# Kernel optimization log

Measured on AMD Instinct MI355X. Metric: run time of the kernel, lower is better.

## Reference

```python
import jax, jax.numpy as jnp
import numpy as np

BN_EPS = 1e-5

def _batchnorm(z, gamma, beta):
    # training-mode BN over node axis, biased variance (matches torch normalization)
    mean = jnp.mean(z, axis=0)
    var = jnp.mean((z - mean) ** 2, axis=0)
    return (z - mean) * jax.lax.rsqrt(var + BN_EPS) * gamma + beta

def setup_inputs() -> dict:
    key = jax.random.key(0)
    N, E, D, L = 100000, 1000000, 128, 2
    ks = jax.random.split(key, 8)
    x = jax.random.normal(ks[0], (N, D), dtype=jnp.float32)
    edge_index = jax.random.randint(ks[1], (2, E), 0, N, dtype=jnp.int64)
    s = 1.0 / np.sqrt(D)
    W1 = jax.random.uniform(ks[2], (L, D, D), jnp.float32, -s, s)
    b1 = jax.random.uniform(ks[3], (L, D), jnp.float32, -s, s)
    W2 = jax.random.uniform(ks[4], (L, D, D), jnp.float32, -s, s)
    b2 = jax.random.uniform(ks[5], (L, D), jnp.float32, -s, s)
    g1 = jnp.ones((L, D), jnp.float32); bt1 = jnp.zeros((L, D), jnp.float32)
    g_out = jnp.ones((L, D), jnp.float32); bt_out = jnp.zeros((L, D), jnp.float32)
    eps = jnp.zeros((L,), jnp.float32)  # GIN eps, init 0
    return {"x": x, "edge_index": edge_index, "W1": W1, "b1": b1, "g1": g1,
            "bt1": bt1, "W2": W2, "b2": b2, "eps": eps, "g_out": g_out, "bt_out": bt_out}

def reference(x, edge_index, W1, b1, g1, bt1, W2, b2, eps, g_out, bt_out):
    N = x.shape[0]
    L = W1.shape[0]
    src, dst = edge_index[0], edge_index[1]
    h = x
    for l in range(L):
        # message: relu(x_j) gathered along edges; aggregate: scatter-add to dst
        msg = jax.nn.relu(h[src])                                  # [E, D]
        aggr = jax.ops.segment_sum(msg, dst, num_segments=N)       # [N, D]
        z = (1.0 + eps[l]) * h + aggr
        # GINConv MLP: Linear -> BN -> ReLU -> Linear
        z = z @ W1[l].T + b1[l]
        z = jax.nn.relu(_batchnorm(z, g1[l], bt1[l]))
        z = z @ W2[l].T + b2[l]
        # outer per-layer BatchNorm
        z = _batchnorm(z, g_out[l], bt_out[l])
        if l < L - 1:
            z = jax.nn.relu(z)
        # dropout is identity in eval mode
        h = z
    return h
```

## Files before the change

kernel.cpp:

```cpp
#include <hip/hip_runtime.h>

typedef unsigned int u32;
typedef unsigned short u16;
typedef __attribute__((ext_vector_type(8))) short bf16x8;
typedef __attribute__((ext_vector_type(4))) float f32x4;

#define DF 128
#define NBUCK 256
#define BUCK_SHIFT 9
#define BUCK_SIZE 512
#define P2_CHUNK 4096
#define NCOPY 16
#define STATW (NCOPY * DF)

__device__ __forceinline__ float bf2f(u32 h) { return __uint_as_float(h << 16); }
__device__ __forceinline__ u16 f2bf(float f) {
  u32 u = __float_as_uint(f);
  u32 r = (u + 0x7fffu + ((u >> 16) & 1u)) >> 16;
  return (u16)r;
}
__device__ __forceinline__ u32 pack2(float a, float b) {
  return (u32)f2bf(a) | ((u32)f2bf(b) << 16);
}

__global__ void k_cvt_f32_bf16(const float* __restrict__ in, u16* __restrict__ out, int n4) {
  int i = blockIdx.x * blockDim.x + threadIdx.x;
  if (i >= n4) return;
  float4 v = ((const float4*)in)[i];
  ((uint2*)out)[i] = make_uint2(pack2(v.x, v.y), pack2(v.z, v.w));
}

__global__ __launch_bounds__(256) void k_p1(const int* __restrict__ dst,
                                            int* __restrict__ bucketCount, int E) {
  __shared__ int h[NBUCK];
  int t = threadIdx.x;
  h[t] = 0;
  __syncthreads();
  for (int e = blockIdx.x * 256 + t; e < E; e += gridDim.x * 256)
    atomicAdd(&h[((u32)dst[e]) >> BUCK_SHIFT], 1);
  __syncthreads();
  if (h[t]) atomicAdd(&bucketCount[t], h[t]);
}

__global__ __launch_bounds__(256) void k_pscan(const int* __restrict__ bucketCount,
                                               int* __restrict__ bucketStart,
                                               int* __restrict__ bucketCursor,
                                               int* __restrict__ rowptr, int N, int E) {
  __shared__ int sh[NBUCK];
  int t = threadIdx.x;
  int c = bucketCount[t];
  sh[t] = c;
  __syncthreads();
  for (int o = 1; o < 256; o <<= 1) {
    int v = (t >= o) ? sh[t - o] : 0;
    __syncthreads();
    sh[t] += v;
    __syncthreads();
  }
  int excl = sh[t] - c;
  bucketStart[t] = excl;
  bucketCursor[t] = excl;
  if (t == 255) { bucketStart[256] = sh[255]; rowptr[N] = E; }
}

__global__ __launch_bounds__(256) void k_p2(const int* __restrict__ src,
                                            const int* __restrict__ dst,
                                            int* __restrict__ bucketCursor,
                                            uint2* __restrict__ part, int E) {
  __shared__ int h[NBUCK], hs[NBUCK], base[NBUCK];
  __shared__ int total;
  __shared__ uint2 buf[P2_CHUNK];
  int t = threadIdx.x;
  int e0 = blockIdx.x * P2_CHUNK;
  h[t] = 0;
  __syncthreads();
  int myb[16], myr[16];
  uint2 mye[16];
  #pragma unroll
  for (int k = 0; k < 16; k++) {
    int e = e0 + k * 256 + t;
    myb[k] = -1;
    if (e < E) {
      int s = src[e], d = dst[e];
      mye[k] = make_uint2((u32)s, (u32)d);
      myb[k] = ((u32)d) >> BUCK_SHIFT;
      myr[k] = atomicAdd(&h[myb[k]], 1);
    }
  }
  __syncthreads();
  int hc = h[t];
  hs[t] = hc;
  __syncthreads();
  for (int o = 1; o < 256; o <<= 1) {
    int v = (t >= o) ? hs[t - o] : 0;
    __syncthreads();
    hs[t] += v;
    __syncthreads();
  }
  if (t == 255) total = hs[255];
  int excl = hs[t] - hc;
  base[t] = hc ? atomicAdd(&bucketCursor[t], hc) : 0;
  __syncthreads();
  hs[t] = excl;
  __syncthreads();
  #pragma unroll
  for (int k = 0; k < 16; k++)
    if (myb[k] >= 0) buf[hs[myb[k]] + myr[k]] = mye[k];
  __syncthreads();
  int tot = total;
  for (int i = t; i < tot; i += 256) {
    uint2 ed = buf[i];
    int b = ed.y >> BUCK_SHIFT;
    part[base[b] + (i - hs[b])] = ed;
  }
}

__global__ __launch_bounds__(256) void k_p3(const uint2* __restrict__ part,
                                            const int* __restrict__ bucketStart,
                                            int* __restrict__ rowptr,
                                            int* __restrict__ adj, int N) {
  __shared__ int deg[BUCK_SIZE], cur[BUCK_SIZE], psum[256];
  int b = blockIdx.x, t = threadIdx.x;
  int nodeBase = b << BUCK_SHIFT;
  int eb = bucketStart[b], ee = bucketStart[b + 1];
  deg[t] = 0; deg[t + 256] = 0;
  __syncthreads();
  for (int e = eb + t; e < ee; e += 256)
    atomicAdd(&deg[(int)part[e].y - nodeBase], 1);
  __syncthreads();
  int a0 = deg[2 * t], a1 = deg[2 * t + 1];
  psum[t] = a0 + a1;
  __syncthreads();
  for (int o = 1; o < 256; o <<= 1) {
    int v = (t >= o) ? psum[t - o] : 0;
    __syncthreads();
    psum[t] += v;
    __syncthreads();
  }
  int basep = psum[t] - (a0 + a1);
  int p0 = eb + basep, p1 = eb + basep + a0;
  cur[2 * t] = p0; cur[2 * t + 1] = p1;
  int n0 = nodeBase + 2 * t, n1 = nodeBase + 2 * t + 1;
  if (n0 < N) rowptr[n0] = p0;
  if (n1 < N) rowptr[n1] = p1;
  __syncthreads();
  for (int e = eb + t; e < ee; e += 256) {
    uint2 ed = part[e];
    int pos = atomicAdd(&cur[(int)ed.y - nodeBase], 1);
    adj[pos] = (int)ed.x;
  }
}

__global__ void k_aggr(const u16* __restrict__ hself, const u16* __restrict__ hmsg,
                       const int* __restrict__ rowptr, const int* __restrict__ adj,
                       const float* __restrict__ epsArr, int layer, int doRelu,
                       u16* __restrict__ z, int N) {
  int wid = (blockIdx.x * blockDim.x + threadIdx.x) >> 6;
  if (wid >= N) return;
  int lane = threadIdx.x & 63;
  int g = lane >> 4, f = lane & 15;
  const uint4* hs4 = (const uint4*)hself;
  const uint4* hm4 = (const uint4*)hmsg;
  float e1 = 1.0f + epsArr[layer];

  float acc[8];
  #pragma unroll
  for (int k = 0; k < 8; k++) acc[k] = 0.0f;

  if (g == 0) {
    uint4 v = hs4[(size_t)wid * 16 + f];
    u32 w[4] = {v.x, v.y, v.z, v.w};
    #pragma unroll
    for (int k = 0; k < 4; k++) {
      acc[2 * k]     = e1 * __uint_as_float(w[k] << 16);
      acc[2 * k + 1] = e1 * __uint_as_float(w[k] & 0xffff0000u);
    }
  }

  int b = rowptr[wid], e = rowptr[wid + 1];
  for (int p = b; p < e; p += 8) {
    int i0 = p + g, i1 = p + 4 + g;
    uint4 v0 = make_uint4(0, 0, 0, 0), v1 = make_uint4(0, 0, 0, 0);
    if (i0 < e) v0 = hm4[(size_t)(u32)adj[i0] * 16 + f];
    if (i1 < e) v1 = hm4[(size_t)(u32)adj[i1] * 16 + f];
    u32 w0[4] = {v0.x, v0.y, v0.z, v0.w};
    u32 w1[4] = {v1.x, v1.y, v1.z, v1.w};
    if (doRelu) {
      #pragma unroll
      for (int k = 0; k < 4; k++) {
        u32 a = w0[k];
        if (a & 0x8000u)     a &= 0xffff0000u;
        if (a & 0x80000000u) a &= 0x0000ffffu;
        w0[k] = a;
        u32 bq = w1[k];
        if (bq & 0x8000u)     bq &= 0xffff0000u;
        if (bq & 0x80000000u) bq &= 0x0000ffffu;
        w1[k] = bq;
      }
    }
    #pragma unroll
    for (int k = 0; k < 4; k++) {
      acc[2 * k]     += __uint_as_float(w0[k] << 16);
      acc[2 * k + 1] += __uint_as_float(w0[k] & 0xffff0000u);
      acc[2 * k]     += __uint_as_float(w1[k] << 16);
      acc[2 * k + 1] += __uint_as_float(w1[k] & 0xffff0000u);
    }
  }

  #pragma unroll
  for (int k = 0; k < 8; k++) {
    acc[k] += __shfl_xor(acc[k], 16);
    acc[k] += __shfl_xor(acc[k], 32);
  }
  if (g == 0) {
    uint4 o = make_uint4(pack2(acc[0], acc[1]), pack2(acc[2], acc[3]),
                         pack2(acc[4], acc[5]), pack2(acc[6], acc[7]));
    ((uint4*)z)[(size_t)wid * 16 + f] = o;
  }
}

__global__ __launch_bounds__(256, 2) void k_gemm(
    const u16* __restrict__ A, const u16* __restrict__ W, const float* __restrict__ bias,
    const float* __restrict__ ain, const float* __restrict__ cin, int trans,
    float* __restrict__ statS, float* __restrict__ statQ,
    u16* __restrict__ out, int Nrows) {
  __shared__ u16 lA[4 * 8 * 64 * 8];
  __shared__ u16 lB[4 * 8 * 64 * 8];
  int tid = threadIdx.x;
  int rowBase = blockIdx.x * 128;

  #pragma unroll
  for (int cc = 0; cc < 8; cc++) {
    int c = tid + cc * 256;
    int lane = c & 63, rt = (c >> 6) & 7, kt = c >> 9;
    int m = lane & 15, quad = lane >> 4;
    int grow = rowBase + rt * 16 + m;
    int gk = kt * 32 + quad * 8;
    uint4 val = make_uint4(0, 0, 0, 0);
    if (grow < Nrows) val = *(const uint4*)(A + (size_t)grow * DF + gk);
    if (trans) {
      float4 av0 = *(const float4*)(ain + gk);
      float4 av1 = *(const float4*)(ain + gk + 4);
      float4 cv0 = *(const float4*)(cin + gk);
      float4 cv1 = *(const float4*)(cin + gk + 4);
      float f0 = fmaxf(fmaf(av0.x, bf2f(val.x & 0xffffu), cv0.x), 0.0f);
      float f1 = fmaxf(fmaf(av0.y, bf2f(val.x >> 16),     cv0.y), 0.0f);
      float f2 = fmaxf(fmaf(av0.z, bf2f(val.y & 0xffffu), cv0.z), 0.0f);
      float f3 = fmaxf(fmaf(av0.w, bf2f(val.y >> 16),     cv0.w), 0.0f);
      float f4 = fmaxf(fmaf(av1.x, bf2f(val.z & 0xffffu), cv1.x), 0.0f);
      float f5 = fmaxf(fmaf(av1.y, bf2f(val.z >> 16),     cv1.y), 0.0f);
      float f6 = fmaxf(fmaf(av1.z, bf2f(val.w & 0xffffu), cv1.z), 0.0f);
      float f7 = fmaxf(fmaf(av1.w, bf2f(val.w >> 16),     cv1.w), 0.0f);
      val = make_uint4(pack2(f0, f1), pack2(f2, f3), pack2(f4, f5), pack2(f6, f7));
    }
    ((uint4*)lA)[c] = val;
  }
  #pragma unroll
  for (int cc = 0; cc < 8; cc++) {
    int c = tid + cc * 256;
    int lane = c & 63, ct = (c >> 6) & 7, kt = c >> 9;
    int n = lane & 15, quad = lane >> 4;
    ((uint4*)lB)[c] = *(const uint4*)(W + (ct * 16 + n) * DF + kt * 32 + quad * 8);
  }
  __syncthreads();

  int lane = tid & 63, w = tid >> 6;
  int rq = w >> 1, cq = w & 1;
  f32x4 acc[4][4];
  #pragma unroll
  for (int i = 0; i < 4; i++)
    #pragma unroll
    for (int j = 0; j < 4; j++) acc[i][j] = (f32x4){0.f, 0.f, 0.f, 0.f};

  const bf16x8* pA = (const bf16x8*)lA;
  const bf16x8* pB = (const bf16x8*)lB;
  #pragma unroll
  for (int kt = 0; kt < 4; kt++) {
    bf16x8 af[4], bfr[4];
    #pragma unroll
    for (int i = 0; i < 4; i++) af[i] = pA[(kt * 8 + rq * 4 + i) * 64 + lane];
    #pragma unroll
    for (int j = 0; j < 4; j++) bfr[j] = pB[(kt * 8 + cq * 4 + j) * 64 + lane];
    #pragma unroll
    for (int i = 0; i < 4; i++)
      #pragma unroll
      for (int j = 0; j < 4; j++)
        acc[i][j] = __builtin_amdgcn_mfma_f32_16x16x32_bf16(af[i], bfr[j], acc[i][j], 0, 0, 0);
  }

  int mcol = lane & 15, quad = lane >> 4;
  float colS[4] = {0, 0, 0, 0}, colQ[4] = {0, 0, 0, 0};
  #pragma unroll
  for (int j = 0; j < 4; j++) {
    int col = (cq * 4 + j) * 16 + mcol;
    float bv = bias[col];
    #pragma unroll
    for (int i = 0; i < 4; i++) {
      int row0 = rowBase + (rq * 4 + i) * 16 + quad * 4;
      #pragma unroll
      for (int r = 0; r < 4; r++) {
        int row = row0 + r;
        if (row < Nrows) {
          float v = acc[i][j][r] + bv;
          out[(size_t)row * DF + col] = f2bf(v);
          colS[j] += v;
          colQ[j] += v * v;
        }
      }
    }
  }
  int copyOff = (blockIdx.x & (NCOPY - 1)) * DF;
  #pragma unroll
  for (int j = 0; j < 4; j++) {
    float s = colS[j], q = colQ[j];
    s += __shfl_xor(s, 16); q += __shfl_xor(q, 16);
    s += __shfl_xor(s, 32); q += __shfl_xor(q, 32);
    if (quad == 0) {
      int col = (cq * 4 + j) * 16 + mcol;
      atomicAdd(&statS[copyOff + col], s);
      atomicAdd(&statQ[copyOff + col], q);
    }
  }
}

__global__ void k_finalize(const float* __restrict__ s, const float* __restrict__ q,
                           const float* __restrict__ gamma, const float* __restrict__ beta,
                           float* __restrict__ a, float* __restrict__ c, int Nrows) {
  int t = threadIdx.x;
  if (t < DF) {
    float S = 0.f, Q = 0.f;
    #pragma unroll
    for (int i = 0; i < NCOPY; i++) { S += s[i * DF + t]; Q += q[i * DF + t]; }
    float inv_n = 1.0f / (float)Nrows;
    float mean = S * inv_n;
    float var = fmaxf(Q * inv_n - mean * mean, 0.0f);
    float iv = rsqrtf(var + 1e-5f);
    float av = gamma[t] * iv;
    a[t] = av;
    c[t] = beta[t] - mean * av;
  }
}

__global__ void k_bnapply_bf16(const u16* __restrict__ u, const float* __restrict__ a,
                               const float* __restrict__ c, u16* __restrict__ h, int n8, int relu) {
  int i = blockIdx.x * blockDim.x + threadIdx.x;
  if (i >= n8) return;
  int col = (i * 8) & 127;
  float4 a0 = *(const float4*)(a + col), a1v = *(const float4*)(a + col + 4);
  float4 c0 = *(const float4*)(c + col), c1v = *(const float4*)(c + col + 4);
  uint4 v = ((const uint4*)u)[i];
  float f0 = fmaf(a0.x, bf2f(v.x & 0xffffu), c0.x);
  float f1 = fmaf(a0.y, bf2f(v.x >> 16),     c0.y);
  float f2 = fmaf(a0.z, bf2f(v.y & 0xffffu), c0.z);
  float f3 = fmaf(a0.w, bf2f(v.y >> 16),     c0.w);
  float f4 = fmaf(a1v.x, bf2f(v.z & 0xffffu), c1v.x);
  float f5 = fmaf(a1v.y, bf2f(v.z >> 16),     c1v.y);
  float f6 = fmaf(a1v.z, bf2f(v.w & 0xffffu), c1v.z);
  float f7 = fmaf(a1v.w, bf2f(v.w >> 16),     c1v.w);
  if (relu) {
    f0 = fmaxf(f0, 0.f); f1 = fmaxf(f1, 0.f); f2 = fmaxf(f2, 0.f); f3 = fmaxf(f3, 0.f);
    f4 = fmaxf(f4, 0.f); f5 = fmaxf(f5, 0.f); f6 = fmaxf(f6, 0.f); f7 = fmaxf(f7, 0.f);
  }
  ((uint4*)h)[i] = make_uint4(pack2(f0, f1), pack2(f2, f3), pack2(f4, f5), pack2(f6, f7));
}

__global__ void k_bnapply_f32(const u16* __restrict__ u, const float* __restrict__ a,
                              const float* __restrict__ c, float* __restrict__ out, int n8) {
  int i = blockIdx.x * blockDim.x + threadIdx.x;
  if (i >= n8) return;
  int col = (i * 8) & 127;
  float4 a0 = *(const float4*)(a + col), a1v = *(const float4*)(a + col + 4);
  float4 c0 = *(const float4*)(c + col), c1v = *(const float4*)(c + col + 4);
  uint4 v = ((const uint4*)u)[i];
  float4 o0, o1;
  o0.x = fmaf(a0.x, bf2f(v.x & 0xffffu), c0.x);
  o0.y = fmaf(a0.y, bf2f(v.x >> 16),     c0.y);
  o0.z = fmaf(a0.z, bf2f(v.y & 0xffffu), c0.z);
  o0.w = fmaf(a0.w, bf2f(v.y >> 16),     c0.w);
  o1.x = fmaf(a1v.x, bf2f(v.z & 0xffffu), c1v.x);
  o1.y = fmaf(a1v.y, bf2f(v.z >> 16),     c1v.y);
  o1.z = fmaf(a1v.z, bf2f(v.w & 0xffffu), c1v.z);
  o1.w = fmaf(a1v.w, bf2f(v.w >> 16),     c1v.w);
  ((float4*)out)[i * 2] = o0;
  ((float4*)out)[i * 2 + 1] = o1;
}

extern "C" void kernel_launch(void* const* d_in, const int* in_sizes, int n_in,
                              void* d_out, int out_size, void* d_ws, size_t ws_size,
                              hipStream_t stream) {
  const float* x    = (const float*)d_in[0];
  const int*   ei   = (const int*)d_in[1];
  const float* W1   = (const float*)d_in[2];
  const float* b1   = (const float*)d_in[3];
  const float* g1   = (const float*)d_in[4];
  const float* bt1  = (const float*)d_in[5];
  const float* W2   = (const float*)d_in[6];
  const float* b2   = (const float*)d_in[7];
  const float* eps  = (const float*)d_in[8];
  const float* gout = (const float*)d_in[9];
  const float* btout= (const float*)d_in[10];

  int N = in_sizes[0] / DF;
  int E = in_sizes[1] / 2;
  int L = in_sizes[8];

  char* ws = (char*)d_ws;
  size_t off = 0;
  auto alloc = [&](size_t bytes) -> void* {
    void* p = ws + off;
    off += (bytes + 255) & ~(size_t)255;
    return p;
  };
  u16* Xb     = (u16*)alloc((size_t)N * DF * 2);
  u16* bufA   = (u16*)alloc((size_t)N * DF * 2);
  u16* bufB   = (u16*)alloc((size_t)N * DF * 2);
  int* rowptr = (int*)alloc((size_t)(N + 1) * 4);
  int* adj    = (int*)alloc((size_t)E * 4);
  uint2* part = (uint2*)alloc((size_t)E * 8);
  int* bCount = (int*)alloc(NBUCK * 4);
  int* bStart = (int*)alloc((NBUCK + 1) * 4);
  int* bCur   = (int*)alloc(NBUCK * 4);
  u16* W1b    = (u16*)alloc((size_t)L * DF * DF * 2);
  u16* W2b    = (u16*)alloc((size_t)L * DF * DF * 2);
  float* stats= (float*)alloc((size_t)L * 4 * STATW * 4);
  float* coefs= (float*)alloc((size_t)L * 4 * DF * 4);

  hipMemsetAsync(bCount, 0, NBUCK * 4, stream);
  hipMemsetAsync(stats, 0, (size_t)L * 4 * STATW * 4, stream);

  int n4x = N * DF / 4;
  k_cvt_f32_bf16<<<(n4x + 255) / 256, 256, 0, stream>>>(x, Xb, n4x);
  int n4w = L * DF * DF / 4;
  k_cvt_f32_bf16<<<(n4w + 255) / 256, 256, 0, stream>>>(W1, W1b, n4w);
  k_cvt_f32_bf16<<<(n4w + 255) / 256, 256, 0, stream>>>(W2, W2b, n4w);

  const int* srcI = ei;
  const int* dstI = ei + E;
  int nbuckets = (N + BUCK_SIZE - 1) >> BUCK_SHIFT;
  k_p1<<<512, 256, 0, stream>>>(dstI, bCount, E);
  k_pscan<<<1, 256, 0, stream>>>(bCount, bStart, bCur, rowptr, N, E);
  k_p2<<<(E + P2_CHUNK - 1) / P2_CHUNK, 256, 0, stream>>>(srcI, dstI, bCur, part, E);
  k_p3<<<nbuckets, 256, 0, stream>>>(part, bStart, rowptr, adj, N);

  int gblocks = (N + 127) / 128;
  int n8 = N * DF / 8;
  for (int l = 0; l < L; l++) {
    float* S1 = stats + (size_t)(l * 4 + 0) * STATW;
    float* Q1 = stats + (size_t)(l * 4 + 1) * STATW;
    float* S2 = stats + (size_t)(l * 4 + 2) * STATW;
    float* Q2 = stats + (size_t)(l * 4 + 3) * STATW;
    float* a1 = coefs + (size_t)(l * 4 + 0) * DF;
    float* c1 = coefs + (size_t)(l * 4 + 1) * DF;
    float* a2 = coefs + (size_t)(l * 4 + 2) * DF;
    float* c2 = coefs + (size_t)(l * 4 + 3) * DF;
    const u16* H = (l == 0) ? Xb : bufB;
    k_aggr<<<(N + 3) / 4, 256, 0, stream>>>(H, H, rowptr, adj, eps, l,
                                            (l == 0) ? 1 : 0, bufA, N);
    k_gemm<<<gblocks, 256, 0, stream>>>(bufA, W1b + l * DF * DF, b1 + l * DF,
                                        nullptr, nullptr, 0, S1, Q1, bufB, N);
    k_finalize<<<1, 128, 0, stream>>>(S1, Q1, g1 + l * DF, bt1 + l * DF, a1, c1, N);
    k_gemm<<<gblocks, 256, 0, stream>>>(bufB, W2b + l * DF * DF, b2 + l * DF,
                                        a1, c1, 1, S2, Q2, bufA, N);
    k_finalize<<<1, 128, 0, stream>>>(S2, Q2, gout + l * DF, btout + l * DF, a2, c2, N);
    if (l < L - 1) {
      k_bnapply_bf16<<<(n8 + 255) / 256, 256, 0, stream>>>(bufA, a2, c2, bufB, n8, 1);
    } else {
      k_bnapply_f32<<<(n8 + 255) / 256, 256, 0, stream>>>(bufA, a2, c2, (float*)d_out, n8);
    }
  }
}
```

Measured before the change: 436.9 us.

## Fuse BN finalize into consumers, drop GEMM LDS staging, merge conversions

The three f32-to-bf16 conversion launches are merged into one kernel. Each block of the downstream GEMM or BN-apply kernel now recomputes the BN coefficients from the partial sums, so the single-block finalize launches go away. The GEMM loads MFMA fragments straight from global memory instead of staging A and W through LDS, and occupancy is raised to 3 blocks. The aggregation accumulators become vector types. This trades launch count and LDS traffic for redundant per-block stat reduction and uncoalesced 16-byte fragment loads from global memory.

New measurement: 449.6 us. 1.03x slower.

```diff
diff --git a/kernel.cpp b/kernel.cpp
--- a/kernel.cpp
+++ b/kernel.cpp
@@ -23,11 +23,18 @@
   return (u32)f2bf(a) | ((u32)f2bf(b) << 16);
 }
 
-__global__ void k_cvt_f32_bf16(const float* __restrict__ in, u16* __restrict__ out, int n4) {
+__global__ void k_cvt3(const float* __restrict__ x, const float* __restrict__ w1,
+                       const float* __restrict__ w2, u16* __restrict__ xb,
+                       u16* __restrict__ w1b, u16* __restrict__ w2b,
+                       int n4x, int n4w) {
   int i = blockIdx.x * blockDim.x + threadIdx.x;
-  if (i >= n4) return;
-  float4 v = ((const float4*)in)[i];
-  ((uint2*)out)[i] = make_uint2(pack2(v.x, v.y), pack2(v.z, v.w));
+  const float* in; u16* out; int idx;
+  if (i < n4x) { in = x; out = xb; idx = i; }
+  else if (i < n4x + n4w) { in = w1; out = w1b; idx = i - n4x; }
+  else if (i < n4x + 2 * n4w) { in = w2; out = w2b; idx = i - n4x - n4w; }
+  else return;
+  float4 v = ((const float4*)in)[idx];
+  ((uint2*)out)[idx] = make_uint2(pack2(v.x, v.y), pack2(v.z, v.w));
 }
 
 __global__ __launch_bounds__(256) void k_p1(const int* __restrict__ dst,
@@ -151,38 +158,34 @@
   }
 }
 
-__global__ void k_aggr(const u16* __restrict__ hself, const u16* __restrict__ hmsg,
-                       const int* __restrict__ rowptr, const int* __restrict__ adj,
-                       const float* __restrict__ epsArr, int layer, int doRelu,
-                       u16* __restrict__ z, int N) {
+__global__ void k_aggr(const u16* __restrict__ h, const int* __restrict__ rowptr,
+                       const int* __restrict__ adj, const float* __restrict__ epsArr,
+                       int layer, int doRelu, u16* __restrict__ z, int N) {
   int wid = (blockIdx.x * blockDim.x + threadIdx.x) >> 6;
   if (wid >= N) return;
   int lane = threadIdx.x & 63;
   int g = lane >> 4, f = lane & 15;
-  const uint4* hs4 = (const uint4*)hself;
-  const uint4* hm4 = (const uint4*)hmsg;
+  const uint4* h4 = (const uint4*)h;
   float e1 = 1.0f + epsArr[layer];
 
-  float acc[8];
-  #pragma unroll
-  for (int k = 0; k < 8; k++) acc[k] = 0.0f;
+  f32x4 accLo = {0.f, 0.f, 0.f, 0.f}, accHi = {0.f, 0.f, 0.f, 0.f};
 
   if (g == 0) {
-    uint4 v = hs4[(size_t)wid * 16 + f];
-    u32 w[4] = {v.x, v.y, v.z, v.w};
-    #pragma unroll
-    for (int k = 0; k < 4; k++) {
-      acc[2 * k]     = e1 * __uint_as_float(w[k] << 16);
-      acc[2 * k + 1] = e1 * __uint_as_float(w[k] & 0xffff0000u);
-    }
+    uint4 v = h4[(size_t)wid * 16 + f];
+    f32x4 lo = {__uint_as_float(v.x << 16), __uint_as_float(v.y << 16),
+                __uint_as_float(v.z << 16), __uint_as_float(v.w << 16)};
+    f32x4 hi = {__uint_as_float(v.x & 0xffff0000u), __uint_as_float(v.y & 0xffff0000u),
+                __uint_as_float(v.z & 0xffff0000u), __uint_as_float(v.w & 0xffff0000u)};
+    accLo = e1 * lo;
+    accHi = e1 * hi;
   }
 
   int b = rowptr[wid], e = rowptr[wid + 1];
   for (int p = b; p < e; p += 8) {
     int i0 = p + g, i1 = p + 4 + g;
     uint4 v0 = make_uint4(0, 0, 0, 0), v1 = make_uint4(0, 0, 0, 0);
-    if (i0 < e) v0 = hm4[(size_t)(u32)adj[i0] * 16 + f];
-    if (i1 < e) v1 = hm4[(size_t)(u32)adj[i1] * 16 + f];
+    if (i0 < e) v0 = h4[(size_t)(u32)adj[i0] * 16 + f];
+    if (i1 < e) v1 = h4[(size_t)(u32)adj[i1] * 16 + f];
     u32 w0[4] = {v0.x, v0.y, v0.z, v0.w};
     u32 w1[4] = {v1.x, v1.y, v1.z, v1.w};
     if (doRelu) {
@@ -198,89 +201,98 @@
         w1[k] = bq;
       }
     }
-    #pragma unroll
-    for (int k = 0; k < 4; k++) {
-      acc[2 * k]     += __uint_as_float(w0[k] << 16);
-      acc[2 * k + 1] += __uint_as_float(w0[k] & 0xffff0000u);
-      acc[2 * k]     += __uint_as_float(w1[k] << 16);
-      acc[2 * k + 1] += __uint_as_float(w1[k] & 0xffff0000u);
-    }
-  }
-
-  #pragma unroll
-  for (int k = 0; k < 8; k++) {
-    acc[k] += __shfl_xor(acc[k], 16);
-    acc[k] += __shfl_xor(acc[k], 32);
+    f32x4 lo0 = {__uint_as_float(w0[0] << 16), __uint_as_float(w0[1] << 16),
+                 __uint_as_float(w0[2] << 16), __uint_as_float(w0[3] << 16)};
+    f32x4 hi0 = {__uint_as_float(w0[0] & 0xffff0000u), __uint_as_float(w0[1] & 0xffff0000u),
+                 __uint_as_float(w0[2] & 0xffff0000u), __uint_as_float(w0[3] & 0xffff0000u)};
+    f32x4 lo1 = {__uint_as_float(w1[0] << 16), __uint_as_float(w1[1] << 16),
+                 __uint_as_float(w1[2] << 16), __uint_as_float(w1[3] << 16)};
+    f32x4 hi1 = {__uint_as_float(w1[0] & 0xffff0000u), __uint_as_float(w1[1] & 0xffff0000u),
+                 __uint_as_float(w1[2] & 0xffff0000u), __uint_as_float(w1[3] & 0xffff0000u)};
+    accLo += lo0; accHi += hi0;
+    accLo += lo1; accHi += hi1;
+  }
+
+  #pragma unroll
+  for (int k = 0; k < 4; k++) {
+    accLo[k] += __shfl_xor(accLo[k], 16);
+    accLo[k] += __shfl_xor(accLo[k], 32);
+    accHi[k] += __shfl_xor(accHi[k], 16);
+    accHi[k] += __shfl_xor(accHi[k], 32);
   }
   if (g == 0) {
-    uint4 o = make_uint4(pack2(acc[0], acc[1]), pack2(acc[2], acc[3]),
-                         pack2(acc[4], acc[5]), pack2(acc[6], acc[7]));
+    uint4 o = make_uint4(pack2(accLo[0], accHi[0]), pack2(accLo[1], accHi[1]),
+                         pack2(accLo[2], accHi[2]), pack2(accLo[3], accHi[3]));
     ((uint4*)z)[(size_t)wid * 16 + f] = o;
   }
 }
 
-__global__ __launch_bounds__(256, 2) void k_gemm(
+__global__ __launch_bounds__(256, 3) void k_gemm(
     const u16* __restrict__ A, const u16* __restrict__ W, const float* __restrict__ bias,
-    const float* __restrict__ ain, const float* __restrict__ cin, int trans,
+    const float* __restrict__ pS, const float* __restrict__ pQ,
+    const float* __restrict__ gamma, const float* __restrict__ beta, int trans,
     float* __restrict__ statS, float* __restrict__ statQ,
     u16* __restrict__ out, int Nrows) {
-  __shared__ u16 lA[4 * 8 * 64 * 8];
-  __shared__ u16 lB[4 * 8 * 64 * 8];
+  __shared__ float sA[DF], sC[DF];
   int tid = threadIdx.x;
-  int rowBase = blockIdx.x * 128;
-
-  #pragma unroll
-  for (int cc = 0; cc < 8; cc++) {
-    int c = tid + cc * 256;
-    int lane = c & 63, rt = (c >> 6) & 7, kt = c >> 9;
-    int m = lane & 15, quad = lane >> 4;
-    int grow = rowBase + rt * 16 + m;
-    int gk = kt * 32 + quad * 8;
-    uint4 val = make_uint4(0, 0, 0, 0);
-    if (grow < Nrows) val = *(const uint4*)(A + (size_t)grow * DF + gk);
-    if (trans) {
-      float4 av0 = *(const float4*)(ain + gk);
-      float4 av1 = *(const float4*)(ain + gk + 4);
-      float4 cv0 = *(const float4*)(cin + gk);
-      float4 cv1 = *(const float4*)(cin + gk + 4);
-      float f0 = fmaxf(fmaf(av0.x, bf2f(val.x & 0xffffu), cv0.x), 0.0f);
-      float f1 = fmaxf(fmaf(av0.y, bf2f(val.x >> 16),     cv0.y), 0.0f);
-      float f2 = fmaxf(fmaf(av0.z, bf2f(val.y & 0xffffu), cv0.z), 0.0f);
-      float f3 = fmaxf(fmaf(av0.w, bf2f(val.y >> 16),     cv0.w), 0.0f);
-      float f4 = fmaxf(fmaf(av1.x, bf2f(val.z & 0xffffu), cv1.x), 0.0f);
-      float f5 = fmaxf(fmaf(av1.y, bf2f(val.z >> 16),     cv1.y), 0.0f);
-      float f6 = fmaxf(fmaf(av1.z, bf2f(val.w & 0xffffu), cv1.z), 0.0f);
-      float f7 = fmaxf(fmaf(av1.w, bf2f(val.w >> 16),     cv1.w), 0.0f);
-      val = make_uint4(pack2(f0, f1), pack2(f2, f3), pack2(f4, f5), pack2(f6, f7));
-    }
-    ((uint4*)lA)[c] = val;
-  }
-  #pragma unroll
-  for (int cc = 0; cc < 8; cc++) {
-    int c = tid + cc * 256;
-    int lane = c & 63, ct = (c >> 6) & 7, kt = c >> 9;
-    int n = lane & 15, quad = lane >> 4;
-    ((uint4*)lB)[c] = *(const uint4*)(W + (ct * 16 + n) * DF + kt * 32 + quad * 8);
-  }
-  __syncthreads();
+  if (trans) {
+    if (tid < DF) {
+      float S = 0.f, Q = 0.f;
+      #pragma unroll
+      for (int i = 0; i < NCOPY; i++) { S += pS[i * DF + tid]; Q += pQ[i * DF + tid]; }
+      float inv_n = 1.0f / (float)Nrows;
+      float mean = S * inv_n;
+      float var = fmaxf(Q * inv_n - mean * mean, 0.0f);
+      float iv = rsqrtf(var + 1e-5f);
+      float av = gamma[tid] * iv;
+      sA[tid] = av;
+      sC[tid] = beta[tid] - mean * av;
+    }
+    __syncthreads();
+  }
 
   int lane = tid & 63, w = tid >> 6;
   int rq = w >> 1, cq = w & 1;
+  int m = lane & 15, quad = lane >> 4;
+  int rowBase = blockIdx.x * 128;
+  int lastRow = Nrows - 1;
+
   f32x4 acc[4][4];
   #pragma unroll
   for (int i = 0; i < 4; i++)
     #pragma unroll
     for (int j = 0; j < 4; j++) acc[i][j] = (f32x4){0.f, 0.f, 0.f, 0.f};
 
-  const bf16x8* pA = (const bf16x8*)lA;
-  const bf16x8* pB = (const bf16x8*)lB;
   #pragma unroll
   for (int kt = 0; kt < 4; kt++) {
+    int gk = kt * 32 + quad * 8;
     bf16x8 af[4], bfr[4];
     #pragma unroll
-    for (int i = 0; i < 4; i++) af[i] = pA[(kt * 8 + rq * 4 + i) * 64 + lane];
-    #pragma unroll
-    for (int j = 0; j < 4; j++) bfr[j] = pB[(kt * 8 + cq * 4 + j) * 64 + lane];
+    for (int i = 0; i < 4; i++) {
+      int row = rowBase + (rq * 4 + i) * 16 + m;
+      row = row < Nrows ? row : lastRow;
+      af[i] = *(const bf16x8*)(A + (size_t)row * DF + gk);
+    }
+    #pragma unroll
+    for (int j = 0; j < 4; j++)
+      bfr[j] = *(const bf16x8*)(W + (size_t)((cq * 4 + j) * 16 + m) * DF + gk);
+    if (trans) {
+      f32x4 a0 = *(const f32x4*)(sA + gk), a1 = *(const f32x4*)(sA + gk + 4);
+      f32x4 c0 = *(const f32x4*)(sC + gk), c1 = *(const f32x4*)(sC + gk + 4);
+      #pragma unroll
+      for (int i = 0; i < 4; i++) {
+        bf16x8 v = af[i];
+        #pragma unroll
+        for (int k = 0; k < 8; k++) {
+          float xk = __uint_as_float(((u32)(u16)v[k]) << 16);
+          float ak = (k < 4) ? a0[k] : a1[k - 4];
+          float ck = (k < 4) ? c0[k] : c1[k - 4];
+          float r = fmaxf(fmaf(ak, xk, ck), 0.0f);
+          v[k] = (short)f2bf(r);
+        }
+        af[i] = v;
+      }
+    }
     #pragma unroll
     for (int i = 0; i < 4; i++)
       #pragma unroll
@@ -288,11 +300,10 @@
         acc[i][j] = __builtin_amdgcn_mfma_f32_16x16x32_bf16(af[i], bfr[j], acc[i][j], 0, 0, 0);
   }
 
-  int mcol = lane & 15, quad = lane >> 4;
   float colS[4] = {0, 0, 0, 0}, colQ[4] = {0, 0, 0, 0};
   #pragma unroll
   for (int j = 0; j < 4; j++) {
-    int col = (cq * 4 + j) * 16 + mcol;
+    int col = (cq * 4 + j) * 16 + m;
     float bv = bias[col];
     #pragma unroll
     for (int i = 0; i < 4; i++) {
@@ -316,71 +327,83 @@
     s += __shfl_xor(s, 16); q += __shfl_xor(q, 16);
     s += __shfl_xor(s, 32); q += __shfl_xor(q, 32);
     if (quad == 0) {
-      int col = (cq * 4 + j) * 16 + mcol;
+      int col = (cq * 4 + j) * 16 + m;
       atomicAdd(&statS[copyOff + col], s);
       atomicAdd(&statQ[copyOff + col], q);
     }
   }
 }
 
-__global__ void k_finalize(const float* __restrict__ s, const float* __restrict__ q,
-                           const float* __restrict__ gamma, const float* __restrict__ beta,
-                           float* __restrict__ a, float* __restrict__ c, int Nrows) {
+__global__ void k_bnapply_bf16(const u16* __restrict__ u, const float* __restrict__ pS,
+                               const float* __restrict__ pQ, const float* __restrict__ gamma,
+                               const float* __restrict__ beta, u16* __restrict__ h,
+                               int n8, int Nrows) {
+  __shared__ float sA[DF], sC[DF];
   int t = threadIdx.x;
   if (t < DF) {
     float S = 0.f, Q = 0.f;
     #pragma unroll
-    for (int i = 0; i < NCOPY; i++) { S += s[i * DF + t]; Q += q[i * DF + t]; }
+    for (int i = 0; i < NCOPY; i++) { S += pS[i * DF + t]; Q += pQ[i * DF + t]; }
     float inv_n = 1.0f / (float)Nrows;
     float mean = S * inv_n;
     float var = fmaxf(Q * inv_n - mean * mean, 0.0f);
     float iv = rsqrtf(var + 1e-5f);
     float av = gamma[t] * iv;
-    a[t] = av;
-    c[t] = beta[t] - mean * av;
-  }
-}
-
-__global__ void k_bnapply_bf16(const u16* __restrict__ u, const float* __restrict__ a,
-                               const float* __restrict__ c, u16* __restrict__ h, int n8, int relu) {
-  int i = blockIdx.x * blockDim.x + threadIdx.x;
+    sA[t] = av;
+    sC[t] = beta[t] - mean * av;
+  }
+  __syncthreads();
+  int i = blockIdx.x * blockDim.x + t;
   if (i >= n8) return;
   int col = (i * 8) & 127;
-  float4 a0 = *(const float4*)(a + col), a1v = *(const float4*)(a + col + 4);
-  float4 c0 = *(const float4*)(c + col), c1v = *(const float4*)(c + col + 4);
+  f32x4 a0 = *(const f32x4*)(sA + col), a1v = *(const f32x4*)(sA + col + 4);
+  f32x4 c0 = *(const f32x4*)(sC + col), c1v = *(const f32x4*)(sC + col + 4);
   uint4 v = ((const uint4*)u)[i];
-  float f0 = fmaf(a0.x, bf2f(v.x & 0xffffu), c0.x);
-  float f1 = fmaf(a0.y, bf2f(v.x >> 16),     c0.y);
-  float f2 = fmaf(a0.z, bf2f(v.y & 0xffffu), c0.z);
-  float f3 = fmaf(a0.w, bf2f(v.y >> 16),     c0.w);
-  float f4 = fmaf(a1v.x, bf2f(v.z & 0xffffu), c1v.x);
-  float f5 = fmaf(a1v.y, bf2f(v.z >> 16),     c1v.y);
-  float f6 = fmaf(a1v.z, bf2f(v.w & 0xffffu), c1v.z);
-  float f7 = fmaf(a1v.w, bf2f(v.w >> 16),     c1v.w);
-  if (relu) {
-    f0 = fmaxf(f0, 0.f); f1 = fmaxf(f1, 0.f); f2 = fmaxf(f2, 0.f); f3 = fmaxf(f3, 0.f);
-    f4 = fmaxf(f4, 0.f); f5 = fmaxf(f5, 0.f); f6 = fmaxf(f6, 0.f); f7 = fmaxf(f7, 0.f);
-  }
+  float f0 = fmaxf(fmaf(a0[0], bf2f(v.x & 0xffffu), c0[0]), 0.f);
+  float f1 = fmaxf(fmaf(a0[1], bf2f(v.x >> 16),     c0[1]), 0.f);
+  float f2 = fmaxf(fmaf(a0[2], bf2f(v.y & 0xffffu), c0[2]), 0.f);
+  float f3 = fmaxf(fmaf(a0[3], bf2f(v.y >> 16),     c0[3]), 0.f);
+  float f4 = fmaxf(fmaf(a1v[0], bf2f(v.z & 0xffffu), c1v[0]), 0.f);
+  float f5 = fmaxf(fmaf(a1v[1], bf2f(v.z >> 16),     c1v[1]), 0.f);
+  float f6 = fmaxf(fmaf(a1v[2], bf2f(v.w & 0xffffu), c1v[2]), 0.f);
+  float f7 = fmaxf(fmaf(a1v[3], bf2f(v.w >> 16),     c1v[3]), 0.f);
   ((uint4*)h)[i] = make_uint4(pack2(f0, f1), pack2(f2, f3), pack2(f4, f5), pack2(f6, f7));
 }
 
-__global__ void k_bnapply_f32(const u16* __restrict__ u, const float* __restrict__ a,
-                              const float* __restrict__ c, float* __restrict__ out, int n8) {
-  int i = blockIdx.x * blockDim.x + threadIdx.x;
+__global__ void k_bnapply_f32(const u16* __restrict__ u, const float* __restrict__ pS,
+                              const float* __restrict__ pQ, const float* __restrict__ gamma,
+                              const float* __restrict__ beta, float* __restrict__ out,
+                              int n8, int Nrows) {
+  __shared__ float sA[DF], sC[DF];
+  int t = threadIdx.x;
+  if (t < DF) {
+    float S = 0.f, Q = 0.f;
+    #pragma unroll
+    for (int i = 0; i < NCOPY; i++) { S += pS[i * DF + t]; Q += pQ[i * DF + t]; }
+    float inv_n = 1.0f / (float)Nrows;
+    float mean = S * inv_n;
+    float var = fmaxf(Q * inv_n - mean * mean, 0.0f);
+    float iv = rsqrtf(var + 1e-5f);
+    float av = gamma[t] * iv;
+    sA[t] = av;
+    sC[t] = beta[t] - mean * av;
+  }
+  __syncthreads();
+  int i = blockIdx.x * blockDim.x + t;
   if (i >= n8) return;
   int col = (i * 8) & 127;
-  float4 a0 = *(const float4*)(a + col), a1v = *(const float4*)(a + col + 4);
-  float4 c0 = *(const float4*)(c + col), c1v = *(const float4*)(c + col + 4);
+  f32x4 a0 = *(const f32x4*)(sA + col), a1v = *(const f32x4*)(sA + col + 4);
+  f32x4 c0 = *(const f32x4*)(sC + col), c1v = *(const f32x4*)(sC + col + 4);
   uint4 v = ((const uint4*)u)[i];
   float4 o0, o1;
-  o0.x = fmaf(a0.x, bf2f(v.x & 0xffffu), c0.x);
-  o0.y = fmaf(a0.y, bf2f(v.x >> 16),     c0.y);
-  o0.z = fmaf(a0.z, bf2f(v.y & 0xffffu), c0.z);
-  o0.w = fmaf(a0.w, bf2f(v.y >> 16),     c0.w);
-  o1.x = fmaf(a1v.x, bf2f(v.z & 0xffffu), c1v.x);
-  o1.y = fmaf(a1v.y, bf2f(v.z >> 16),     c1v.y);
-  o1.z = fmaf(a1v.z, bf2f(v.w & 0xffffu), c1v.z);
-  o1.w = fmaf(a1v.w, bf2f(v.w >> 16),     c1v.w);
+  o0.x = fmaf(a0[0], bf2f(v.x & 0xffffu), c0[0]);
+  o0.y = fmaf(a0[1], bf2f(v.x >> 16),     c0[1]);
+  o0.z = fmaf(a0[2], bf2f(v.y & 0xffffu), c0[2]);
+  o0.w = fmaf(a0[3], bf2f(v.y >> 16),     c0[3]);
+  o1.x = fmaf(a1v[0], bf2f(v.z & 0xffffu), c1v[0]);
+  o1.y = fmaf(a1v[1], bf2f(v.z >> 16),     c1v[1]);
+  o1.z = fmaf(a1v[2], bf2f(v.w & 0xffffu), c1v[2]);
+  o1.w = fmaf(a1v[3], bf2f(v.w >> 16),     c1v[3]);
   ((float4*)out)[i * 2] = o0;
   ((float4*)out)[i * 2 + 1] = o1;
 }
@@ -423,16 +446,14 @@
   u16* W1b    = (u16*)alloc((size_t)L * DF * DF * 2);
   u16* W2b    = (u16*)alloc((size_t)L * DF * DF * 2);
   float* stats= (float*)alloc((size_t)L * 4 * STATW * 4);
-  float* coefs= (float*)alloc((size_t)L * 4 * DF * 4);
 
   hipMemsetAsync(bCount, 0, NBUCK * 4, stream);
   hipMemsetAsync(stats, 0, (size_t)L * 4 * STATW * 4, stream);
 
   int n4x = N * DF / 4;
-  k_cvt_f32_bf16<<<(n4x + 255) / 256, 256, 0, stream>>>(x, Xb, n4x);
   int n4w = L * DF * DF / 4;
-  k_cvt_f32_bf16<<<(n4w + 255) / 256, 256, 0, stream>>>(W1, W1b, n4w);
-  k_cvt_f32_bf16<<<(n4w + 255) / 256, 256, 0, stream>>>(W2, W2b, n4w);
+  int n4tot = n4x + 2 * n4w;
+  k_cvt3<<<(n4tot + 255) / 256, 256, 0, stream>>>(x, W1, W2, Xb, W1b, W2b, n4x, n4w);
 
   const int* srcI = ei;
   const int* dstI = ei + E;
@@ -449,23 +470,21 @@
     float* Q1 = stats + (size_t)(l * 4 + 1) * STATW;
     float* S2 = stats + (size_t)(l * 4 + 2) * STATW;
     float* Q2 = stats + (size_t)(l * 4 + 3) * STATW;
-    float* a1 = coefs + (size_t)(l * 4 + 0) * DF;
-    float* c1 = coefs + (size_t)(l * 4 + 1) * DF;
-    float* a2 = coefs + (size_t)(l * 4 + 2) * DF;
-    float* c2 = coefs + (size_t)(l * 4 + 3) * DF;
     const u16* H = (l == 0) ? Xb : bufB;
-    k_aggr<<<(N + 3) / 4, 256, 0, stream>>>(H, H, rowptr, adj, eps, l,
+    k_aggr<<<(N + 3) / 4, 256, 0, stream>>>(H, rowptr, adj, eps, l,
                                             (l == 0) ? 1 : 0, bufA, N);
     k_gemm<<<gblocks, 256, 0, stream>>>(bufA, W1b + l * DF * DF, b1 + l * DF,
-                                        nullptr, nullptr, 0, S1, Q1, bufB, N);
-    k_finalize<<<1, 128, 0, stream>>>(S1, Q1, g1 + l * DF, bt1 + l * DF, a1, c1, N);
+                                        nullptr, nullptr, nullptr, nullptr, 0,
+                                        S1, Q1, bufB, N);
     k_gemm<<<gblocks, 256, 0, stream>>>(bufB, W2b + l * DF * DF, b2 + l * DF,
-                                        a1, c1, 1, S2, Q2, bufA, N);
-    k_finalize<<<1, 128, 0, stream>>>(S2, Q2, gout + l * DF, btout + l * DF, a2, c2, N);
+                                        S1, Q1, g1 + l * DF, bt1 + l * DF, 1,
+                                        S2, Q2, bufA, N);
     if (l < L - 1) {
-      k_bnapply_bf16<<<(n8 + 255) / 256, 256, 0, stream>>>(bufA, a2, c2, bufB, n8, 1);
+      k_bnapply_bf16<<<(n8 + 255) / 256, 256, 0, stream>>>(
+          bufA, S2, Q2, gout + l * DF, btout + l * DF, bufB, n8, N);
     } else {
-      k_bnapply_f32<<<(n8 + 255) / 256, 256, 0, stream>>>(bufA, a2, c2, (float*)d_out, n8);
-    }
-  }
-}
+      k_bnapply_f32<<<(n8 + 255) / 256, 256, 0, stream>>>(
+          bufA, S2, Q2, gout + l * DF, btout + l * DF, (float*)d_out, n8, N);
+    }
+  }
+}
```
